# Performance work log

Measured on AMD Instinct MI355X. Metric: run time of the kernel, lower is better.

The kernel has to match this reference:

```python
import jax, jax.numpy as jnp
import numpy as np

B, T, D = 32, 1024, 512   # batch, encoder length, listener feature dim (= speller hidden)
H = 512                   # speller_hidden_dim
V = 64                    # output_class_dim
S = 128                   # max_label_len (decode steps, no teacher forcing)


def setup_inputs() -> dict:
    key = jax.random.key(0)
    ks = jax.random.split(key, 7)
    s = lambda n: 1.0 / np.sqrt(n)
    return {
        "listener_feature": jax.random.normal(ks[0], (B, T, D), jnp.float32),
        "W_ih": jax.random.normal(ks[1], (4 * H, V + H), jnp.float32) * s(V + H),
        "W_hh": jax.random.normal(ks[2], (4 * H, H), jnp.float32) * s(H),
        "b_ih": jax.random.normal(ks[3], (4 * H,), jnp.float32) * 0.01,
        "b_hh": jax.random.normal(ks[4], (4 * H,), jnp.float32) * 0.01,
        "W_out": jax.random.normal(ks[5], (V, 2 * H), jnp.float32) * s(2 * H),
        "b_out": jax.random.normal(ks[6], (V,), jnp.float32) * 0.01,
    }


def reference(listener_feature, W_ih, W_hh, b_ih, b_hh, W_out, b_out):
    Bb = listener_feature.shape[0]

    def step(carry, _):
        h, c, x = carry                              # h,c: [B,H]; x: [B,V+H]
        gates = x @ W_ih.T + b_ih + h @ W_hh.T + b_hh  # [B,4H], torch gate order i,f,g,o
        i, f, g, o = jnp.split(gates, 4, axis=-1)
        i = jax.nn.sigmoid(i); f = jax.nn.sigmoid(f)
        g = jnp.tanh(g);       o = jax.nn.sigmoid(o)
        c = f * c + i * g
        h = o * jnp.tanh(c)                          # rnn_output [B,H]
        # dot attention over listener features
        energy = jnp.einsum('bd,btd->bt', h, listener_feature)   # [B,T]
        attn = jax.nn.softmax(energy, axis=-1)
        ctx = jnp.einsum('bt,btd->bd', attn, listener_feature)   # [B,D]
        concat = jnp.concatenate([h, ctx], axis=-1)              # [B,2H]
        logp = jax.nn.log_softmax(concat @ W_out.T + b_out, axis=-1)  # [B,V]
        # decode_mode == 1: greedy one-hot feedback (non-differentiable argmax)
        ow = jax.nn.one_hot(jnp.argmax(logp, axis=-1), V, dtype=logp.dtype)
        x_next = jnp.concatenate([ow, ctx], axis=-1)
        return (h, c, x_next), (logp, attn)

    # initial word = one-hot of class 0; first rnn input concatenates listener_feature[:,0,:]
    ow0 = jnp.zeros((Bb, V), listener_feature.dtype).at[:, 0].set(1.0)
    x0 = jnp.concatenate([ow0, listener_feature[:, 0, :]], axis=-1)
    h0 = jnp.zeros((Bb, H), listener_feature.dtype)
    c0 = jnp.zeros((Bb, H), listener_feature.dtype)

    _, (raw_pred_seq, attention_record) = jax.lax.scan(step, (h0, c0, x0), None, length=S)
    return raw_pred_seq, attention_record   # [S,B,V], [S,B,T]
```

## Files before the change

### kernel.cpp

```cpp
#include <hip/hip_runtime.h>

#define Bn 32
#define Tn 1024
#define Dn 512
#define Hn 512
#define Vn 64
#define Sn 128
#define NTS 8
#define TT 128
#define NTHREADS 512
#define KIH 576
#define NBLK 256

#define LDS_BYTES 143360
#define OUT_ATT ((size_t)Sn * Bn * Vn)

#define WS_XCTX  1024
#define WS_XH    17408
#define WS_LGP   50176
#define WS_MST   66560
#define WS_LST   66816
#define WS_CTXP  67072

struct F8 { float4 a, b; };

__device__ __forceinline__ float bfu(unsigned short u){ return __uint_as_float(((unsigned int)u)<<16); }
__device__ __forceinline__ float bflo(unsigned int u){ return __uint_as_float(u<<16); }
__device__ __forceinline__ float bfhi(unsigned int u){ return __uint_as_float(u & 0xffff0000u); }
__device__ __forceinline__ unsigned short f2bf(float f){
  unsigned int x = __float_as_uint(f);
  return (unsigned short)((x + 0x7fffu + ((x>>16)&1u)) >> 16);
}
__device__ __forceinline__ F8 ld8(const unsigned short* p){
  uint4 q = *(const uint4*)p;
  F8 r;
  r.a = make_float4(bflo(q.x), bfhi(q.x), bflo(q.y), bfhi(q.y));
  r.b = make_float4(bflo(q.z), bfhi(q.z), bflo(q.w), bfhi(q.w));
  return r;
}
__device__ __forceinline__ F8 ld8(const float* p){
  F8 r; r.a = *(const float4*)p; r.b = *(const float4*)(p+4); return r;
}
__device__ __forceinline__ float dot8(F8 w, float4 a, float4 b){
  return w.a.x*a.x + w.a.y*a.y + w.a.z*a.z + w.a.w*a.w
       + w.b.x*b.x + w.b.y*b.y + w.b.z*b.z + w.b.w*b.w;
}
__device__ __forceinline__ float dot64g(const unsigned short* __restrict__ w, const float* x){
  const float4* x4 = (const float4*)x;
  float acc = 0.f;
#pragma unroll
  for(int i=0;i<8;i++) acc += dot8(ld8(w+8*i), x4[2*i], x4[2*i+1]);
  return acc;
}
__device__ __forceinline__ float sigm(float x){
  x = fminf(fmaxf(x, -30.f), 30.f); return 1.f/(1.f + expf(-x));
}
__device__ __forceinline__ float tnh(float x){
  return tanhf(fminf(fmaxf(x, -20.f), 20.f));
}

template<int N>
__device__ __forceinline__ void rs_round(float* a, int off, bool hi){
#pragma unroll
  for(int i=0;i<N;i++){
    float send = hi ? a[i]   : a[i+N];
    float keep = hi ? a[i+N] : a[i];
    float recv = __shfl_xor(send, off);
    a[i] = keep + recv;
  }
}
__device__ __forceinline__ void rs32(float* a, int lane){
  rs_round<16>(a, 32, (lane&32)!=0);
  rs_round< 8>(a, 16, (lane&16)!=0);
  rs_round< 4>(a,  8, (lane& 8)!=0);
  rs_round< 2>(a,  4, (lane& 4)!=0);
  rs_round< 1>(a,  2, (lane& 2)!=0);
  a[0] += __shfl_xor(a[0], 1);
}

__device__ __forceinline__ void aput(float* p, float v){
  __hip_atomic_store(p, v, __ATOMIC_RELAXED, __HIP_MEMORY_SCOPE_AGENT);
}
__device__ __forceinline__ float aget(const float* p){
  return __hip_atomic_load(p, __ATOMIC_RELAXED, __HIP_MEMORY_SCOPE_AGENT);
}
__device__ __forceinline__ unsigned int uget(const unsigned int* p){
  return __hip_atomic_load(p, __ATOMIC_RELAXED, __HIP_MEMORY_SCOPE_AGENT);
}

template<bool ACQ>
__device__ __forceinline__ void gbar2(unsigned int* wsu, unsigned int ggen){
  asm volatile("s_waitcnt vmcnt(0)" ::: "memory");
  __syncthreads();
  const int tid = threadIdx.x;
  const int grp = (int)blockIdx.x >> 3;
  if(tid == 0)
    __hip_atomic_fetch_add(&wsu[grp*16], 1u, __ATOMIC_RELEASE, __HIP_MEMORY_SCOPE_AGENT);
  if(tid < 64){
    const unsigned int tgt = 8u*ggen;
    for(;;){
      unsigned int v = (tid < 32) ? uget(&wsu[tid*16]) : tgt;
      if(__all(v >= tgt)) break;
      __builtin_amdgcn_s_sleep(1);
    }
    if(ACQ && tid == 0){
      unsigned int x = __hip_atomic_load(&wsu[grp*16], __ATOMIC_ACQUIRE, __HIP_MEMORY_SCOPE_AGENT);
      asm volatile("" :: "v"(x));
    }
  }
  __syncthreads();
  asm volatile("" ::: "memory");
}

__device__ __forceinline__ void gbarE(unsigned int* line){
  asm volatile("s_waitcnt vmcnt(0)" ::: "memory");
  __syncthreads();
  if(threadIdx.x == 0){
    unsigned int g = uget(line+1);
    unsigned int p = __hip_atomic_fetch_add(line, 1u, __ATOMIC_RELEASE, __HIP_MEMORY_SCOPE_AGENT);
    if(p == g*8u + 7u){
      __hip_atomic_store(line+1, g+1u, __ATOMIC_RELEASE, __HIP_MEMORY_SCOPE_AGENT);
    } else {
      while(uget(line+1) == g) __builtin_amdgcn_s_sleep(1);
    }
  }
  __syncthreads();
  asm volatile("" ::: "memory");
}

__global__ void dtype_probe(const unsigned short* __restrict__ b3, unsigned int* flag){
  const int t = threadIdx.x;
  bool ok = true;
#pragma unroll
  for(int i=0;i<8;i++){
    float v = bfu(b3[2*(t*8+i)]);
    ok = ok && (v == v) && (fabsf(v) < 0.5f);
  }
  unsigned long long m = __ballot(ok);
  if(t == 0)
    __hip_atomic_store(flag, (m == ~0ull) ? 1u : 2u, __ATOMIC_RELEASE, __HIP_MEMORY_SCOPE_AGENT);
}

__global__ __launch_bounds__(NTHREADS, 1)
void speller_v3(const float* __restrict__ lf,  const float* __restrict__ wih,
                const float* __restrict__ whh, const float* __restrict__ bih,
                const float* __restrict__ bhh, const float* __restrict__ wout,
                const float* __restrict__ bout, float* __restrict__ out,
                float* __restrict__ ws)
{
  { unsigned int fl = __hip_atomic_load((unsigned int*)ws + 512, __ATOMIC_ACQUIRE, __HIP_MEMORY_SCOPE_AGENT);
    if(fl != 2u) return; }

  const int tid   = threadIdx.x;
  const int UP    = (int)blockIdx.x;
  const int b_att = UP >> 3;
  const int ts    = UP & 7;
  const int w     = tid >> 6;
  const int lane  = tid & 63;

  extern __shared__ char smem[];
  float* tile   = (float*)smem;
  float* epart  = (float*)(smem + 131072);
  float* h_s    = epart + 512;
  float* e_s    = h_s + 512;
  float* p_s    = e_s + 128;
  float* red_s  = p_s + 128;
  float* pre_s  = red_s + 32;
  float* ctxc_s = pre_s + 256;
  float* c_s    = ctxc_s + 64;
  float* bias_s = c_s + 64;
  float* bout_s = bias_s + 8;
  int*   pall_s = (int*)(bout_s + 64);
  float* wow_s  = (float*)(pall_s + 32);

  unsigned int* wsu   = (unsigned int*)ws;
  unsigned int* eline = wsu + (size_t)b_att*16 + 4;
  float* xctx = ws + WS_XCTX;
  float* xh   = ws + WS_XH;
  float* lgp  = ws + WS_LGP;
  float* mst  = ws + WS_MST;
  float* lst  = ws + WS_LST;
  float* ctxp = ws + WS_CTXP;

  const int rw = (w>>1)*Hn + 2*UP + (w&1);

  float4 wv0, wv1, wv2, wv3;
  {
    const int k0 = 16*lane;
    const float* wp = (lane < 32) ? (wih + (size_t)rw*KIH + 64 + k0)
                                  : (whh + (size_t)rw*Hn + (k0 - 512));
    wv0 = *(const float4*)wp;     wv1 = *(const float4*)(wp+4);
    wv2 = *(const float4*)(wp+8); wv3 = *(const float4*)(wp+12);
  }
  float4 oh0, oh1, oc0, oc1;
  {
    const int v = tid>>3, q = tid&7;
    const float* pH = wout + (size_t)v*(2*Hn) + ts*64 + q*8;
    const float* pC = pH + Hn;
    oh0 = *(const float4*)pH; oh1 = *(const float4*)(pH+4);
    oc0 = *(const float4*)pC; oc1 = *(const float4*)(pC+4);
  }

  {
    const int rr = tid>>6, cc = tid&63;
    const int r2 = (rr>>1)*Hn + 2*UP + (rr&1);
    wow_s[tid] = wih[(size_t)r2*KIH + cc];
  }
  if(tid < 8){ const int r2 = (tid>>1)*Hn + 2*UP + (tid&1); bias_s[tid] = bih[r2] + bhh[r2]; }
  if(tid < Vn) bout_s[tid] = bout[tid];
  if(tid < 64) c_s[tid] = 0.f;
  if(tid < 32) pall_s[tid] = 0;

  float lfreg[64];
  {
    const float4* s4 = (const float4*)(lf + ((size_t)b_att*Tn + (size_t)ts*TT) * Dn);
    float4* d4 = (float4*)tile;
#pragma unroll
    for(int i=0;i<16;i++){
      const int f = tid + i*NTHREADS;
      const int row = f >> 7, cc = f & 127;
      d4[(row << 7) | (cc ^ (row & 7))] = s4[f];
    }
    const float* lfg = lf + ((size_t)b_att*Tn + (size_t)ts*TT + 64) * Dn + tid;
#pragma unroll
    for(int j=0;j<64;j++) lfreg[j] = lfg[(size_t)j*Dn];
  }

  if(tid < 64){
    aput(&xctx[(size_t)b_att*Dn + ts*64 + tid], lf[(size_t)b_att*Tn*Dn + ts*64 + tid]);
    const int bb = tid>>1, ul = tid&1;
    aput(&xh[(size_t)Bn*Hn + (size_t)bb*Hn + 2*UP + ul], 0.f);
  }
  __syncthreads();
  unsigned int gg = 0;
  gbar2<true>(wsu, ++gg);

  for(int s = 0; s <= Sn; ++s){
    if(s > 0){
      for(int ii=0; ii<4; ++ii){
        const int bb = 4*w + ii;
        float lv = bout_s[lane];
        const float4* lp = (const float4*)(lgp + ((size_t)bb*Vn + lane)*8);
        float4 qa = lp[0], qb = lp[1];
        lv += qa.x+qa.y+qa.z+qa.w + qb.x+qb.y+qb.z+qb.w;
        float mv = lv; int mi = lane;
#pragma unroll
        for(int off=1; off<64; off<<=1){
          float ov = __shfl_xor(mv, off);
          int   oi = __shfl_xor(mi, off);
          if(ov > mv || (ov == mv && oi < mi)){ mv = ov; mi = oi; }
        }
        float se = expf(lv - mv);
#pragma unroll
        for(int off=1; off<64; off<<=1) se += __shfl_xor(se, off);
        if(lane == 0) pall_s[bb] = mi;
        if(UP == 8*bb) out[((size_t)(s-1)*Bn + bb)*Vn + lane] = lv - mv - logf(se);
      }
    }
    if(s == Sn) break;
    __syncthreads();

    {
      const float* xhR = xh + (size_t)(((s+1)&1))*Bn*Hn;
      const int k0 = 16*lane;
      const float* xbase = (lane < 32) ? (xctx + k0) : (xhR + (k0 - 512));
      float acc[Bn];
#pragma unroll
      for(int bb=0; bb<Bn; ++bb){
        const float4* xp = (const float4*)(xbase + (size_t)bb*Dn);
        float4 x0 = xp[0], x1 = xp[1], x2 = xp[2], x3 = xp[3];
        acc[bb] = wv0.x*x0.x + wv0.y*x0.y + wv0.z*x0.z + wv0.w*x0.w
                + wv1.x*x1.x + wv1.y*x1.y + wv1.z*x1.z + wv1.w*x1.w
                + wv2.x*x2.x + wv2.y*x2.y + wv2.z*x2.z + wv2.w*x2.w
                + wv3.x*x3.x + wv3.y*x3.y + wv3.z*x3.z + wv3.w*x3.w;
      }
      rs32(acc, lane);
      if((lane & 1) == 0) pre_s[w*Bn + (lane>>1)] = acc[0];
    }
    __syncthreads();
    if(tid < 64){
      const int bb = tid>>1, ul = tid&1;
      const int pidx = pall_s[bb];
      float gi = sigm(pre_s[(0+ul)*Bn+bb] + wow_s[(0+ul)*64+pidx] + bias_s[0+ul]);
      float gf = sigm(pre_s[(2+ul)*Bn+bb] + wow_s[(2+ul)*64+pidx] + bias_s[2+ul]);
      float gg2 = tnh(pre_s[(4+ul)*Bn+bb] + wow_s[(4+ul)*64+pidx] + bias_s[4+ul]);
      float go = sigm(pre_s[(6+ul)*Bn+bb] + wow_s[(6+ul)*64+pidx] + bias_s[6+ul]);
      float c = gf*c_s[tid] + gi*gg2;
      c_s[tid] = c;
      aput(&xh[(size_t)(s&1)*Bn*Hn + (size_t)bb*Hn + 2*UP + ul], go*tnh(c));
    }
    gbar2<false>(wsu, ++gg);

    h_s[tid] = aget(&xh[(size_t)(s&1)*Bn*Hn + (size_t)b_att*Hn + tid]);
    __syncthreads();
    {
      const int t1 = tid >> 3, q = tid & 7, mm = t1 & 7;
      const float4* lrow = (const float4*)tile + (size_t)t1*128;
      const float4* hq = (const float4*)(h_s + q*64);
      float ea = 0.f;
#pragma unroll
      for(int i=0;i<8;i++){
        const int c0 = q*16 + 2*i;
        F8 wv; wv.a = lrow[c0 ^ mm]; wv.b = lrow[(c0+1) ^ mm];
        ea += dot8(wv, hq[2*i], hq[2*i+1]);
      }
#pragma unroll
      for(int off=1; off<8; off<<=1) ea += __shfl_xor(ea, off);
      if(q==0) e_s[t1] = ea;
    }
    {
      const float h_own = h_s[tid];
      float a[32];
#pragma unroll
      for(int j=0;j<32;j++) a[j] = h_own * lfreg[j];
      rs32(a, lane);
      if((lane & 1) == 0) epart[(w<<6) + (lane>>1)] = a[0];
#pragma unroll
      for(int j=0;j<32;j++) a[j] = h_own * lfreg[32+j];
      rs32(a, lane);
      if((lane & 1) == 0) epart[(w<<6) + 32 + (lane>>1)] = a[0];
    }
    __syncthreads();
    if(tid < 64){
      float s2 = 0.f;
#pragma unroll
      for(int w2=0; w2<8; w2++) s2 += epart[(w2<<6) + tid];
      e_s[64 + tid] = s2;
      float v = fmaxf(e_s[tid], s2);
#pragma unroll
      for(int off=1; off<64; off<<=1) v = fmaxf(v, __shfl_xor(v,off));
      if(tid==0) red_s[10] = v;
    }
    __syncthreads();
    if(tid < TT) p_s[tid] = expf(e_s[tid] - red_s[10]);
    __syncthreads();
    if(tid < 64){
      float v = p_s[tid] + p_s[tid+64];
#pragma unroll
      for(int off=1; off<64; off<<=1) v += __shfl_xor(v,off);
      if(tid==0){
        aput(&mst[(size_t)b_att*NTS + ts], red_s[10]);
        aput(&lst[(size_t)b_att*NTS + ts], v);
      }
    }
    {
      float acc = 0.f;
      const int cs = tid >> 2, cr = tid & 3;
#pragma unroll
      for(int t=0;t<64;t++)
        acc += p_s[t] * tile[(size_t)t*Dn + (((cs ^ (t&7))<<2) | cr)];
#pragma unroll
      for(int j=0;j<64;j++) acc += p_s[64+j] * lfreg[j];
      aput(&ctxp[((size_t)b_att*NTS + ts)*Dn + tid], acc);
    }
    gbarE(eline);

    if(tid < NTS){
      red_s[16+tid] = aget(&mst[(size_t)b_att*NTS + tid]);
      red_s[24+tid] = aget(&lst[(size_t)b_att*NTS + tid]);
    }
    __syncthreads();
    if(tid == 0){
      float m = -3.0e38f;
#pragma unroll
      for(int j=0;j<NTS;j++) m = fmaxf(m, red_s[16+j]);
      float l = 0.f;
#pragma unroll
      for(int j=0;j<NTS;j++){ float fac = expf(red_s[16+j]-m); red_s[j]=fac; l += fac*red_s[24+j]; }
      red_s[8]=m; red_s[9]=l;
    }
    __syncthreads();
    {
      const float gm = red_s[8];
      const float gl = red_s[9];
      if(tid < TT)
        out[OUT_ATT + ((size_t)s*Bn + b_att)*Tn + (size_t)ts*TT + tid] = expf(e_s[tid] - gm)/gl;
      if(tid < 64){
        const int d = ts*64 + tid;
        float acc = 0.f;
#pragma unroll
        for(int j=0;j<NTS;j++) acc += red_s[j] * aget(&ctxp[((size_t)b_att*NTS + j)*Dn + d]);
        const float cv = acc / gl;
        ctxc_s[tid] = cv;
        aput(&xctx[(size_t)b_att*Dn + d], cv);
      }
    }
    __syncthreads();
    {
      const int v = tid>>3, q = tid&7;
      const float4* hp = (const float4*)(h_s + ts*64 + q*8);
      const float4* cp = (const float4*)(ctxc_s + q*8);
      float4 ha = hp[0], hb = hp[1], ca = cp[0], cb = cp[1];
      float acc = oh0.x*ha.x + oh0.y*ha.y + oh0.z*ha.z + oh0.w*ha.w
                + oh1.x*hb.x + oh1.y*hb.y + oh1.z*hb.z + oh1.w*hb.w
                + oc0.x*ca.x + oc0.y*ca.y + oc0.z*ca.z + oc0.w*ca.w
                + oc1.x*cb.x + oc1.y*cb.y + oc1.z*cb.z + oc1.w*cb.w;
#pragma unroll
      for(int off=1; off<8; off<<=1) acc += __shfl_xor(acc, off);
      if(q == 0) aput(&lgp[((size_t)b_att*Vn + v)*8 + ts], acc);
    }
    gbar2<true>(wsu, ++gg);
  }
}

__device__ __forceinline__ void gbar8(unsigned int* bar){
  asm volatile("s_waitcnt vmcnt(0)" ::: "memory");
  __syncthreads();
  if(threadIdx.x==0){
    unsigned int g = uget(bar+1);
    unsigned int p = __hip_atomic_fetch_add(bar, 1u, __ATOMIC_RELAXED, __HIP_MEMORY_SCOPE_AGENT);
    if(p == g*NTS + (NTS-1)){
      __hip_atomic_store(bar+1, g+1u, __ATOMIC_RELAXED, __HIP_MEMORY_SCOPE_AGENT);
    } else {
      while(uget(bar+1) == g) __builtin_amdgcn_s_sleep(2);
    }
  }
  __syncthreads();
  asm volatile("" ::: "memory");
}

__global__ __launch_bounds__(NTHREADS, 2)
void speller_bf16(const unsigned short* __restrict__ lf, const unsigned short* __restrict__ wih,
                  const unsigned short* __restrict__ whh, const unsigned short* __restrict__ bih,
                  const unsigned short* __restrict__ bhh, const unsigned short* __restrict__ wout,
                  const unsigned short* __restrict__ bout, unsigned short* __restrict__ out,
                  float* __restrict__ ws)
{
  { unsigned int fl = __hip_atomic_load((unsigned int*)ws + 512, __ATOMIC_ACQUIRE, __HIP_MEMORY_SCOPE_AGENT);
    if(fl != 1u) return; }
  const int tid = threadIdx.x;
  const int b   = (int)(blockIdx.x >> 3);
  const int ts  = (int)(blockIdx.x & 7);

  extern __shared__ char smem[];
  unsigned short* lf_s = (unsigned short*)smem;
  float* h_s   = (float*)(smem + 131072);
  float* ctx_s = h_s + 512;
  float* e_s   = ctx_s + 512;
  float* p_s   = e_s + 128;
  float* lg_s  = p_s + 128;
  float* red_s = lg_s + 64;
  float* c_s   = red_s + 32;
  int*   i_s   = (int*)(c_s + 64);

  unsigned int* bar = (unsigned int*)ws + (size_t)b*16 + 4;
  float* hbuf = ws + 1024  + (size_t)b*Hn;
  float* mstB = ws + WS_MST + (size_t)b*NTS;
  float* lstB = ws + WS_LST + (size_t)b*NTS;
  float* ctxpB= ws + WS_CTXP + (size_t)b*NTS*Dn;

  {
    const uint4* s4 = (const uint4*)(lf + ((size_t)b*Tn + (size_t)ts*TT) * Dn);
    uint4* d4 = (uint4*)lf_s;
#pragma unroll
    for(int i=0;i<16;i++) d4[tid + i*NTHREADS] = s4[tid + i*NTHREADS];
  }
  h_s[tid] = 0.f;
  if(tid < 64) c_s[tid] = 0.f;
  if(tid == 0) i_s[0] = 0;
  __syncthreads();

  for(int s = 0; s <= Sn; ++s){
    if(s > 0){
      if(tid < NTS){ red_s[16+tid] = aget(&mstB[tid]); red_s[24+tid] = aget(&lstB[tid]); }
      __syncthreads();
      if(tid == 0){
        float m = -3.0e38f;
#pragma unroll
        for(int j=0;j<NTS;j++) m = fmaxf(m, red_s[16+j]);
        float l = 0.f;
#pragma unroll
        for(int j=0;j<NTS;j++){ float fac = expf(red_s[16+j]-m); red_s[j]=fac; l += fac*red_s[24+j]; }
        red_s[8]=m; red_s[9]=l;
      }
      __syncthreads();
      const float gm = red_s[8];
      const float gl = red_s[9];
      {
        float acc = 0.f;
#pragma unroll
        for(int j=0;j<NTS;j++) acc += red_s[j] * aget(&ctxpB[(size_t)j*Dn + tid]);
        ctx_s[tid] = acc / gl;
      }
      if(tid < TT)
        out[OUT_ATT + ((size_t)(s-1)*Bn + b)*Tn + (size_t)ts*TT + tid] = f2bf(expf(e_s[tid]-gm)/gl);
      __syncthreads();
      {
        const int j = tid >> 3, ks = tid & 7;
        const unsigned short* wr = wout + (size_t)j*(2*Hn) + ks*128;
        float acc;
        if(ks < 4) acc = dot64g(wr, h_s + ks*128)       + dot64g(wr+64, h_s + ks*128 + 64);
        else       acc = dot64g(wr, ctx_s + (ks-4)*128) + dot64g(wr+64, ctx_s + (ks-4)*128 + 64);
#pragma unroll
        for(int off=1; off<8; off<<=1) acc += __shfl_xor(acc, off);
        if(ks==0) lg_s[j] = acc + bfu(bout[j]);
      }
      __syncthreads();
      if(tid < Vn){
        const float lv = lg_s[tid];
        float mv = lv; int mi = tid;
#pragma unroll
        for(int off=1; off<64; off<<=1){
          float ov = __shfl_xor(mv, off);
          int   oi = __shfl_xor(mi, off);
          if(ov > mv || (ov == mv && oi < mi)){ mv = ov; mi = oi; }
        }
        float se = expf(lv - mv);
#pragma unroll
        for(int off=1; off<64; off<<=1) se += __shfl_xor(se, off);
        if(ts == 0) out[((size_t)(s-1)*Bn + b)*Vn + tid] = f2bf(lv - mv - logf(se));
        if(tid == 0) i_s[0] = mi;
      }
      __syncthreads();
    } else {
      ctx_s[tid] = bfu(lf[(size_t)b*Tn*Dn + tid]);
      __syncthreads();
    }

    if(s == Sn) break;

    {
      const int u  = tid >> 3;
      const int ks = tid & 7;
      const int uu = ts*64 + u;
      const unsigned short* wi0 = wih + (size_t)(       uu)*KIH + 64 + ks*64;
      const unsigned short* wi1 = wih + (size_t)(  Hn + uu)*KIH + 64 + ks*64;
      const unsigned short* wi2 = wih + (size_t)(2*Hn + uu)*KIH + 64 + ks*64;
      const unsigned short* wi3 = wih + (size_t)(3*Hn + uu)*KIH + 64 + ks*64;
      const unsigned short* wh0 = whh + (size_t)(       uu)*Hn + ks*64;
      const unsigned short* wh1 = whh + (size_t)(  Hn + uu)*Hn + ks*64;
      const unsigned short* wh2 = whh + (size_t)(2*Hn + uu)*Hn + ks*64;
      const unsigned short* wh3 = whh + (size_t)(3*Hn + uu)*Hn + ks*64;
      const float4* xc = (const float4*)(ctx_s + ks*64);
      const float4* xh4 = (const float4*)(h_s   + ks*64);
      float a0=0.f,a1=0.f,a2=0.f,a3=0.f;
#pragma unroll
      for(int i=0;i<8;i++){
        float4 p0 = xc[2*i], p1 = xc[2*i+1];
        a0 += dot8(ld8(wi0+8*i), p0, p1);
        a1 += dot8(ld8(wi1+8*i), p0, p1);
        a2 += dot8(ld8(wi2+8*i), p0, p1);
        a3 += dot8(ld8(wi3+8*i), p0, p1);
      }
#pragma unroll
      for(int i=0;i<8;i++){
        float4 p0 = xh4[2*i], p1 = xh4[2*i+1];
        a0 += dot8(ld8(wh0+8*i), p0, p1);
        a1 += dot8(ld8(wh1+8*i), p0, p1);
        a2 += dot8(ld8(wh2+8*i), p0, p1);
        a3 += dot8(ld8(wh3+8*i), p0, p1);
      }
#pragma unroll
      for(int off=1; off<8; off<<=1){
        a0 += __shfl_xor(a0, off);
        a1 += __shfl_xor(a1, off);
        a2 += __shfl_xor(a2, off);
        a3 += __shfl_xor(a3, off);
      }
      if(ks == 0){
        const int pidx = i_s[0];
        const int r0 = uu, r1 = Hn+uu, r2 = 2*Hn+uu, r3 = 3*Hn+uu;
        float gi = a0 + bfu(wih[(size_t)r0*KIH + pidx]) + bfu(bih[r0]) + bfu(bhh[r0]);
        float gf = a1 + bfu(wih[(size_t)r1*KIH + pidx]) + bfu(bih[r1]) + bfu(bhh[r1]);
        float gg = a2 + bfu(wih[(size_t)r2*KIH + pidx]) + bfu(bih[r2]) + bfu(bhh[r2]);
        float go = a3 + bfu(wih[(size_t)r3*KIH + pidx]) + bfu(bih[r3]) + bfu(bhh[r3]);
        gi = sigm(gi); gf = sigm(gf); gg = tnh(gg); go = sigm(go);
        float c = gf*c_s[u] + gi*gg;
        c_s[u] = c;
        aput(&hbuf[uu], go * tnh(c));
      }
    }
    gbar8(bar);

    h_s[tid] = aget(&hbuf[tid]);
    __syncthreads();
    {
      const int t2 = tid >> 3;
      const int q  = tid & 7;
      const float4* hq = (const float4*)(h_s + q*64);
      float ea=0.f, eb=0.f;
      const unsigned short* la = lf_s + (size_t)(2*t2  )*Dn + q*64;
      const unsigned short* lb = lf_s + (size_t)(2*t2+1)*Dn + q*64;
#pragma unroll
      for(int i=0;i<8;i++){
        float4 p0 = hq[2*i], p1 = hq[2*i+1];
        ea += dot8(ld8(la+8*i), p0, p1);
        eb += dot8(ld8(lb+8*i), p0, p1);
      }
#pragma unroll
      for(int off=1; off<8; off<<=1){ ea += __shfl_xor(ea,off); eb += __shfl_xor(eb,off); }
      if(q==0){ e_s[2*t2] = ea; e_s[2*t2+1] = eb; }
    }
    __syncthreads();
    if(tid < 64){
      float v = fmaxf(e_s[tid], e_s[tid+64]);
#pragma unroll
      for(int off=1; off<64; off<<=1) v = fmaxf(v, __shfl_xor(v,off));
      if(tid==0) red_s[10] = v;
    }
    __syncthreads();
    if(tid < TT) p_s[tid] = expf(e_s[tid] - red_s[10]);
    __syncthreads();
    if(tid < 64){
      float v = p_s[tid] + p_s[tid+64];
#pragma unroll
      for(int off=1; off<64; off<<=1) v += __shfl_xor(v,off);
      if(tid==0){ aput(&mstB[ts], red_s[10]); aput(&lstB[ts], v); }
    }
    {
      float acc = 0.f;
      const unsigned short* col = lf_s + tid;
#pragma unroll 4
      for(int t=0;t<TT;t++) acc += p_s[t] * bfu(col[(size_t)t*Dn]);
      aput(&ctxpB[(size_t)ts*Dn + tid], acc);
    }
    gbar8(bar);
  }
}

extern "C" void kernel_launch(void* const* d_in, const int* in_sizes, int n_in,
                              void* d_out, int out_size, void* d_ws, size_t ws_size,
                              hipStream_t stream) {
  (void)in_sizes; (void)n_in; (void)out_size; (void)ws_size;
  float* ws = (float*)d_ws;

  hipFuncSetAttribute(reinterpret_cast<const void*>(&speller_v3),
                      hipFuncAttributeMaxDynamicSharedMemorySize, LDS_BYTES);
  hipFuncSetAttribute(reinterpret_cast<const void*>(&speller_bf16),
                      hipFuncAttributeMaxDynamicSharedMemorySize, LDS_BYTES);
  hipMemsetAsync(d_ws, 0, 4096, stream);
  dtype_probe<<<dim3(1), dim3(64), 0, stream>>>((const unsigned short*)d_in[3],
                                                (unsigned int*)d_ws + 512);
  speller_v3<<<dim3(NBLK), dim3(NTHREADS), LDS_BYTES, stream>>>(
      (const float*)d_in[0], (const float*)d_in[1], (const float*)d_in[2],
      (const float*)d_in[3], (const float*)d_in[4], (const float*)d_in[5],
      (const float*)d_in[6], (float*)d_out, ws);
  speller_bf16<<<dim3(NBLK), dim3(NTHREADS), LDS_BYTES, stream>>>(
      (const unsigned short*)d_in[0], (const unsigned short*)d_in[1],
      (const unsigned short*)d_in[2], (const unsigned short*)d_in[3],
      (const unsigned short*)d_in[4], (const unsigned short*)d_in[5],
      (const unsigned short*)d_in[6], (unsigned short*)d_out, ws);
}
```

Measured before the change: 6.851 ms.

## Double fp32 speller block size to 1024 threads, splitting per-thread work

Launches the fp32 persistent speller kernel with 1024 threads per block instead of 512. Each thread now handles half the gate dot-product slice, half the register-held listener rows, and half the output-projection slice, with extra LDS partial sums for the gate and context reductions. The aim is to cut per-thread serial work and register pressure in each latency-bound decode step by using more waves per CU. The cost is extra LDS traffic, an additional block-wide sync for the context reduction, and heavier __syncthreads and grid barriers with twice the threads.

Measured after the change: 8.810 ms. 28.6% more time.

```diff
diff --git a/kernel.cpp b/kernel.cpp
--- a/kernel.cpp
+++ b/kernel.cpp
@@ -9,10 +9,11 @@
 #define NTS 8
 #define TT 128
 #define NTHREADS 512
+#define NT2 1024
 #define KIH 576
 #define NBLK 256
 
-#define LDS_BYTES 143360
+#define LDS_BYTES 147456
 #define OUT_ATT ((size_t)Sn * Bn * Vn)
 
 #define WS_XCTX  1024
@@ -44,6 +45,9 @@
 __device__ __forceinline__ float dot8(F8 w, float4 a, float4 b){
   return w.a.x*a.x + w.a.y*a.y + w.a.z*a.z + w.a.w*a.w
        + w.b.x*b.x + w.b.y*b.y + w.b.z*b.z + w.b.w*b.w;
+}
+__device__ __forceinline__ float dot4(float4 w, float4 a){
+  return w.x*a.x + w.y*a.y + w.z*a.z + w.w*a.w;
 }
 __device__ __forceinline__ float dot64g(const unsigned short* __restrict__ w, const float* x){
   const float4* x4 = (const float4*)x;
@@ -141,7 +145,7 @@
     __hip_atomic_store(flag, (m == ~0ull) ? 1u : 2u, __ATOMIC_RELEASE, __HIP_MEMORY_SCOPE_AGENT);
 }
 
-__global__ __launch_bounds__(NTHREADS, 1)
+__global__ __launch_bounds__(NT2, 1)
 void speller_v3(const float* __restrict__ lf,  const float* __restrict__ wih,
                 const float* __restrict__ whh, const float* __restrict__ bih,
                 const float* __restrict__ bhh, const float* __restrict__ wout,
@@ -160,18 +164,19 @@
 
   extern __shared__ char smem[];
   float* tile   = (float*)smem;
-  float* epart  = (float*)(smem + 131072);
-  float* h_s    = epart + 512;
+  float* epart2 = (float*)(smem + 131072);
+  float* h_s    = epart2 + 512;
   float* e_s    = h_s + 512;
   float* p_s    = e_s + 128;
   float* red_s  = p_s + 128;
-  float* pre_s  = red_s + 32;
-  float* ctxc_s = pre_s + 256;
+  float* pre2_s = red_s + 32;
+  float* ctxc_s = pre2_s + 512;
   float* c_s    = ctxc_s + 64;
   float* bias_s = c_s + 64;
   float* bout_s = bias_s + 8;
   int*   pall_s = (int*)(bout_s + 64);
   float* wow_s  = (float*)(pall_s + 32);
+  float* ctxp2_s= wow_s + 512;
 
   unsigned int* wsu   = (unsigned int*)ws;
   unsigned int* eline = wsu + (size_t)b_att*16 + 4;
@@ -182,26 +187,24 @@
   float* lst  = ws + WS_LST;
   float* ctxp = ws + WS_CTXP;
 
-  const int rw = (w>>1)*Hn + 2*UP + (w&1);
-
-  float4 wv0, wv1, wv2, wv3;
+  const int rl  = w >> 1;
+  const int hf2 = w & 1;
+  const int rw  = (rl>>1)*Hn + 2*UP + (rl&1);
+
+  float4 wv0, wv1;
   {
-    const int k0 = 16*lane;
-    const float* wp = (lane < 32) ? (wih + (size_t)rw*KIH + 64 + k0)
-                                  : (whh + (size_t)rw*Hn + (k0 - 512));
-    wv0 = *(const float4*)wp;     wv1 = *(const float4*)(wp+4);
-    wv2 = *(const float4*)(wp+8); wv3 = *(const float4*)(wp+12);
-  }
-  float4 oh0, oh1, oc0, oc1;
+    const float* wp = (hf2 == 0) ? (wih + (size_t)rw*KIH + 64 + 8*lane)
+                                 : (whh + (size_t)rw*Hn + 8*lane);
+    wv0 = ((const float4*)wp)[0]; wv1 = ((const float4*)wp)[1];
+  }
+  float4 oh, oc;
   {
-    const int v = tid>>3, q = tid&7;
-    const float* pH = wout + (size_t)v*(2*Hn) + ts*64 + q*8;
-    const float* pC = pH + Hn;
-    oh0 = *(const float4*)pH; oh1 = *(const float4*)(pH+4);
-    oc0 = *(const float4*)pC; oc1 = *(const float4*)(pC+4);
-  }
-
-  {
+    const int v = tid>>4, q = tid&15;
+    oh = *(const float4*)(wout + (size_t)v*(2*Hn) + ts*64 + q*4);
+    oc = *(const float4*)(wout + (size_t)v*(2*Hn) + Hn + ts*64 + q*4);
+  }
+
+  if(tid < 512){
     const int rr = tid>>6, cc = tid&63;
     const int r2 = (rr>>1)*Hn + 2*UP + (rr&1);
     wow_s[tid] = wih[(size_t)r2*KIH + cc];
@@ -211,19 +214,20 @@
   if(tid < 64) c_s[tid] = 0.f;
   if(tid < 32) pall_s[tid] = 0;
 
-  float lfreg[64];
+  float lfreg[32];
+  const int col = tid & 511, gB = tid >> 9;
   {
     const float4* s4 = (const float4*)(lf + ((size_t)b_att*Tn + (size_t)ts*TT) * Dn);
     float4* d4 = (float4*)tile;
 #pragma unroll
-    for(int i=0;i<16;i++){
-      const int f = tid + i*NTHREADS;
+    for(int i=0;i<8;i++){
+      const int f = tid + i*NT2;
       const int row = f >> 7, cc = f & 127;
       d4[(row << 7) | (cc ^ (row & 7))] = s4[f];
     }
-    const float* lfg = lf + ((size_t)b_att*Tn + (size_t)ts*TT + 64) * Dn + tid;
-#pragma unroll
-    for(int j=0;j<64;j++) lfreg[j] = lfg[(size_t)j*Dn];
+    const float* lfg = lf + ((size_t)b_att*Tn + (size_t)ts*TT + 64 + gB*32) * Dn + col;
+#pragma unroll
+    for(int j=0;j<32;j++) lfreg[j] = lfg[(size_t)j*Dn];
   }
 
   if(tid < 64){
@@ -237,8 +241,8 @@
 
   for(int s = 0; s <= Sn; ++s){
     if(s > 0){
-      for(int ii=0; ii<4; ++ii){
-        const int bb = 4*w + ii;
+      for(int ii=0; ii<2; ++ii){
+        const int bb = 2*w + ii;
         float lv = bout_s[lane];
         const float4* lp = (const float4*)(lgp + ((size_t)bb*Vn + lane)*8);
         float4 qa = lp[0], qb = lp[1];
@@ -262,69 +266,71 @@
 
     {
       const float* xhR = xh + (size_t)(((s+1)&1))*Bn*Hn;
-      const int k0 = 16*lane;
-      const float* xbase = (lane < 32) ? (xctx + k0) : (xhR + (k0 - 512));
+      const float* xbase = (hf2 == 0) ? (xctx + 8*lane) : (xhR + 8*lane);
       float acc[Bn];
 #pragma unroll
       for(int bb=0; bb<Bn; ++bb){
         const float4* xp = (const float4*)(xbase + (size_t)bb*Dn);
-        float4 x0 = xp[0], x1 = xp[1], x2 = xp[2], x3 = xp[3];
+        float4 x0 = xp[0], x1 = xp[1];
         acc[bb] = wv0.x*x0.x + wv0.y*x0.y + wv0.z*x0.z + wv0.w*x0.w
-                + wv1.x*x1.x + wv1.y*x1.y + wv1.z*x1.z + wv1.w*x1.w
-                + wv2.x*x2.x + wv2.y*x2.y + wv2.z*x2.z + wv2.w*x2.w
-                + wv3.x*x3.x + wv3.y*x3.y + wv3.z*x3.z + wv3.w*x3.w;
+                + wv1.x*x1.x + wv1.y*x1.y + wv1.z*x1.z + wv1.w*x1.w;
       }
       rs32(acc, lane);
-      if((lane & 1) == 0) pre_s[w*Bn + (lane>>1)] = acc[0];
+      if((lane & 1) == 0) pre2_s[w*32 + (lane>>1)] = acc[0];
     }
     __syncthreads();
     if(tid < 64){
       const int bb = tid>>1, ul = tid&1;
       const int pidx = pall_s[bb];
-      float gi = sigm(pre_s[(0+ul)*Bn+bb] + wow_s[(0+ul)*64+pidx] + bias_s[0+ul]);
-      float gf = sigm(pre_s[(2+ul)*Bn+bb] + wow_s[(2+ul)*64+pidx] + bias_s[2+ul]);
-      float gg2 = tnh(pre_s[(4+ul)*Bn+bb] + wow_s[(4+ul)*64+pidx] + bias_s[4+ul]);
-      float go = sigm(pre_s[(6+ul)*Bn+bb] + wow_s[(6+ul)*64+pidx] + bias_s[6+ul]);
+      float pg[4];
+#pragma unroll
+      for(int g2=0; g2<4; ++g2){
+        const int rloc = 2*g2 + ul;
+        pg[g2] = pre2_s[(2*rloc)*32 + bb] + pre2_s[(2*rloc+1)*32 + bb]
+               + wow_s[rloc*64 + pidx] + bias_s[rloc];
+      }
+      float gi = sigm(pg[0]);
+      float gf = sigm(pg[1]);
+      float gg2 = tnh(pg[2]);
+      float go = sigm(pg[3]);
       float c = gf*c_s[tid] + gi*gg2;
       c_s[tid] = c;
       aput(&xh[(size_t)(s&1)*Bn*Hn + (size_t)bb*Hn + 2*UP + ul], go*tnh(c));
     }
     gbar2<false>(wsu, ++gg);
 
-    h_s[tid] = aget(&xh[(size_t)(s&1)*Bn*Hn + (size_t)b_att*Hn + tid]);
-    __syncthreads();
-    {
-      const int t1 = tid >> 3, q = tid & 7, mm = t1 & 7;
+    if(tid < 512) h_s[tid] = aget(&xh[(size_t)(s&1)*Bn*Hn + (size_t)b_att*Hn + tid]);
+    __syncthreads();
+    {
+      const int t1 = tid >> 4, q = tid & 15, mm = t1 & 7;
       const float4* lrow = (const float4*)tile + (size_t)t1*128;
-      const float4* hq = (const float4*)(h_s + q*64);
+      const float4* hq = (const float4*)(h_s + q*32);
       float ea = 0.f;
 #pragma unroll
-      for(int i=0;i<8;i++){
-        const int c0 = q*16 + 2*i;
-        F8 wv; wv.a = lrow[c0 ^ mm]; wv.b = lrow[(c0+1) ^ mm];
-        ea += dot8(wv, hq[2*i], hq[2*i+1]);
-      }
-#pragma unroll
-      for(int off=1; off<8; off<<=1) ea += __shfl_xor(ea, off);
+      for(int i=0;i<4;i++){
+        const int ir = (i + q) & 3;
+        const int c0 = q*8 + 2*ir;
+        F8 wvv; wvv.a = lrow[c0 ^ mm]; wvv.b = lrow[(c0+1) ^ mm];
+        ea += dot8(wvv, hq[2*ir], hq[2*ir+1]);
+      }
+#pragma unroll
+      for(int off=1; off<16; off<<=1) ea += __shfl_xor(ea, off);
       if(q==0) e_s[t1] = ea;
     }
     {
-      const float h_own = h_s[tid];
+      const float h_own = h_s[col];
       float a[32];
 #pragma unroll
       for(int j=0;j<32;j++) a[j] = h_own * lfreg[j];
       rs32(a, lane);
-      if((lane & 1) == 0) epart[(w<<6) + (lane>>1)] = a[0];
-#pragma unroll
-      for(int j=0;j<32;j++) a[j] = h_own * lfreg[32+j];
-      rs32(a, lane);
-      if((lane & 1) == 0) epart[(w<<6) + 32 + (lane>>1)] = a[0];
+      if((lane & 1) == 0) epart2[w*32 + (lane>>1)] = a[0];
     }
     __syncthreads();
     if(tid < 64){
+      const int gb = tid>>5, i2 = tid&31;
       float s2 = 0.f;
 #pragma unroll
-      for(int w2=0; w2<8; w2++) s2 += epart[(w2<<6) + tid];
+      for(int k=0;k<8;k++) s2 += epart2[(gb*8 + k)*32 + i2];
       e_s[64 + tid] = s2;
       float v = fmaxf(e_s[tid], s2);
 #pragma unroll
@@ -345,14 +351,20 @@
     }
     {
       float acc = 0.f;
-      const int cs = tid >> 2, cr = tid & 3;
-#pragma unroll
-      for(int t=0;t<64;t++)
+      const int cs = col >> 2, cr = col & 3;
+      const int t0 = gB*32;
+#pragma unroll
+      for(int t2=0;t2<32;t2++){
+        const int t = t0 + t2;
         acc += p_s[t] * tile[(size_t)t*Dn + (((cs ^ (t&7))<<2) | cr)];
-#pragma unroll
-      for(int j=0;j<64;j++) acc += p_s[64+j] * lfreg[j];
-      aput(&ctxp[((size_t)b_att*NTS + ts)*Dn + tid], acc);
-    }
+      }
+#pragma unroll
+      for(int j=0;j<32;j++) acc += p_s[64 + gB*32 + j] * lfreg[j];
+      ctxp2_s[gB*512 + col] = acc;
+    }
+    __syncthreads();
+    if(tid < 512)
+      aput(&ctxp[((size_t)b_att*NTS + ts)*Dn + tid], ctxp2_s[tid] + ctxp2_s[512 + tid]);
     gbarE(eline);
 
     if(tid < NTS){
@@ -387,16 +399,12 @@
     }
     __syncthreads();
     {
-      const int v = tid>>3, q = tid&7;
-      const float4* hp = (const float4*)(h_s + ts*64 + q*8);
-      const float4* cp = (const float4*)(ctxc_s + q*8);
-      float4 ha = hp[0], hb = hp[1], ca = cp[0], cb = cp[1];
-      float acc = oh0.x*ha.x + oh0.y*ha.y + oh0.z*ha.z + oh0.w*ha.w
-                + oh1.x*hb.x + oh1.y*hb.y + oh1.z*hb.z + oh1.w*hb.w
-                + oc0.x*ca.x + oc0.y*ca.y + oc0.z*ca.z + oc0.w*ca.w
-                + oc1.x*cb.x + oc1.y*cb.y + oc1.z*cb.z + oc1.w*cb.w;
-#pragma unroll
-      for(int off=1; off<8; off<<=1) acc += __shfl_xor(acc, off);
+      const int v = tid>>4, q = tid&15;
+      float4 ha = *(const float4*)(h_s + ts*64 + q*4);
+      float4 ca = *(const float4*)(ctxc_s + q*4);
+      float acc = dot4(oh, ha) + dot4(oc, ca);
+#pragma unroll
+      for(int off=1; off<16; off<<=1) acc += __shfl_xor(acc, off);
       if(q == 0) aput(&lgp[((size_t)b_att*Vn + v)*8 + ts], acc);
     }
     gbar2<true>(wsu, ++gg);
@@ -631,7 +639,7 @@
   hipMemsetAsync(d_ws, 0, 4096, stream);
   dtype_probe<<<dim3(1), dim3(64), 0, stream>>>((const unsigned short*)d_in[3],
                                                 (unsigned int*)d_ws + 512);
-  speller_v3<<<dim3(NBLK), dim3(NTHREADS), LDS_BYTES, stream>>>(
+  speller_v3<<<dim3(NBLK), dim3(NT2), LDS_BYTES, stream>>>(
       (const float*)d_in[0], (const float*)d_in[1], (const float*)d_in[2],
       (const float*)d_in[3], (const float*)d_in[4], (const float*)d_in[5],
       (const float*)d_in[6], (float*)d_out, ws);
```
